# Performance work log

Hardware: AMD Instinct MI355X
Metric: run time of the kernel (lower is better)

The kernel has to match this reference:

```python
import jax, jax.numpy as jnp
import numpy as np

N = 10000      # nodes
E = 160000     # edges
F_IN = 128     # input_dim
HID = 128      # hidden_dim = per-head channels (concat=False)
OUT = 128      # output_dim
H = 4          # heads
L = 4          # layers (all 128->128 here, so params stack)


def setup_inputs() -> dict:
    key = jax.random.key(0)
    ks = jax.random.split(key, 12)
    x = jax.random.normal(ks[0], (N, F_IN), dtype=jnp.float32)
    edge_index = jax.random.randint(ks[1], (2, E), 0, N, dtype=jnp.int64)
    s = 1.0 / np.sqrt(F_IN)
    Wq = jax.random.normal(ks[2], (L, F_IN, H * HID), dtype=jnp.float32) * s
    bq = jnp.zeros((L, H * HID), dtype=jnp.float32)
    Wk = jax.random.normal(ks[3], (L, F_IN, H * HID), dtype=jnp.float32) * s
    bk = jnp.zeros((L, H * HID), dtype=jnp.float32)
    Wv = jax.random.normal(ks[4], (L, F_IN, H * HID), dtype=jnp.float32) * s
    bv = jnp.zeros((L, H * HID), dtype=jnp.float32)
    Wskip = jax.random.normal(ks[5], (L, F_IN, HID), dtype=jnp.float32) * s
    bskip = jnp.zeros((L, HID), dtype=jnp.float32)
    return {"x": x, "edge_index": edge_index, "Wq": Wq, "bq": bq,
            "Wk": Wk, "bk": bk, "Wv": Wv, "bv": bv,
            "Wskip": Wskip, "bskip": bskip}


def _transformer_conv(x, src, dst, Wq, bq, Wk, bk, Wv, bv, Ws, bs):
    # PyG TransformerConv, concat=False (mean over heads), root_weight=True
    n = x.shape[0]
    q = (x @ Wq + bq).reshape(n, H, HID)
    k = (x @ Wk + bk).reshape(n, H, HID)
    v = (x @ Wv + bv).reshape(n, H, HID)
    # per-edge attention logits: [E, H]
    alpha = jnp.einsum('ehc,ehc->eh', q[dst], k[src]) / jnp.sqrt(jnp.float32(HID))
    # segment softmax over destination node
    m = jax.ops.segment_max(alpha, dst, num_segments=n)          # [N, H]
    e = jnp.exp(alpha - m[dst])                                  # [E, H]
    z = jax.ops.segment_sum(e, dst, num_segments=n)              # [N, H]
    a = e / z[dst]                                               # [E, H]
    msg = a[:, :, None] * v[src]                                 # [E, H, C]
    out = jax.ops.segment_sum(msg, dst, num_segments=n)          # [N, H, C]
    out = out.mean(axis=1)                                       # concat=False
    return out + x @ Ws + bs                                     # skip (root_weight)


def reference(x, edge_index, Wq, bq, Wk, bk, Wv, bv, Wskip, bskip):
    src = edge_index[0]
    dst = edge_index[1]
    h = x
    for l in range(L - 1):
        h = _transformer_conv(h, src, dst, Wq[l], bq[l], Wk[l], bk[l],
                              Wv[l], bv[l], Wskip[l], bskip[l])
        h = jax.nn.relu(h)  # dropout p in eval/reference is identity
    h = _transformer_conv(h, src, dst, Wq[-1], bq[-1], Wk[-1], bk[-1],
                          Wv[-1], bv[-1], Wskip[-1], bskip[-1])
    return h
```

## Files before the change

### kernel.cpp

```cpp
#include <hip/hip_runtime.h>
#include <math.h>

static constexpr int F  = 128;
static constexpr int H  = 4;
static constexpr int HF = 512;
static constexpr int NCP = 640;
static constexpr int LAYERS = 4;

typedef __attribute__((ext_vector_type(8))) short bf16x8;
typedef __attribute__((ext_vector_type(4))) float f32x4;

__device__ __forceinline__ unsigned short f2bf(float f) {
    union { float f; unsigned u; } v; v.f = f;
    unsigned r = (v.u + 0x7FFFu + ((v.u >> 16) & 1u)) >> 16;
    return (unsigned short)r;
}
__device__ __forceinline__ float bf2f(unsigned short b) {
    union { unsigned u; float f; } v; v.u = ((unsigned)b) << 16;
    return v.f;
}

__device__ __forceinline__ float row16_sum(float x) {
    int t;
    t = __builtin_amdgcn_update_dpp(0, __float_as_int(x), 0xB1, 0xF, 0xF, true);
    x += __int_as_float(t);
    t = __builtin_amdgcn_update_dpp(0, __float_as_int(x), 0x4E, 0xF, 0xF, true);
    x += __int_as_float(t);
    t = __builtin_amdgcn_update_dpp(0, __float_as_int(x), 0x124, 0xF, 0xF, true);
    x += __int_as_float(t);
    t = __builtin_amdgcn_update_dpp(0, __float_as_int(x), 0x128, 0xF, 0xF, true);
    x += __int_as_float(t);
    return x;
}

__global__ void hist_kernel(const int* __restrict__ dst, int* __restrict__ deg, int E) {
    int e = blockIdx.x * blockDim.x + threadIdx.x;
    if (e < E) atomicAdd(&deg[dst[e]], 1);
}

__global__ void scan_kernel(const int* __restrict__ deg, int* __restrict__ row_ptr, int n) {
    __shared__ int wsum[16];
    __shared__ int carry_s, wtot_s;
    const int tid = threadIdx.x;
    const int lane = tid & 63;
    const int wid = tid >> 6;
    if (tid == 0) { carry_s = 0; row_ptr[0] = 0; }
    __syncthreads();
    for (int base = 0; base < n; base += 1024) {
        int i = base + tid;
        int x = (i < n) ? deg[i] : 0;
#pragma unroll
        for (int off = 1; off < 64; off <<= 1) {
            int t = __shfl_up(x, off, 64);
            if (lane >= off) x += t;
        }
        if (lane == 63) wsum[wid] = x;
        __syncthreads();
        if (tid == 0) {
            int s = 0;
#pragma unroll
            for (int j = 0; j < 16; ++j) { int t = wsum[j]; wsum[j] = s; s += t; }
            wtot_s = s;
        }
        __syncthreads();
        int incl = x + wsum[wid] + carry_s;
        if (i < n) row_ptr[i + 1] = incl;
        __syncthreads();
        if (tid == 0) carry_s += wtot_s;
        __syncthreads();
    }
}

__global__ void scatter_kernel(const int* __restrict__ src, const int* __restrict__ dst,
                               const int* __restrict__ row_ptr, int* __restrict__ cursor,
                               int* __restrict__ csr_src, int E) {
    int e = blockIdx.x * blockDim.x + threadIdx.x;
    if (e < E) {
        int d = dst[e];
        int pos = atomicAdd(&cursor[d], 1);
        csr_src[row_ptr[d] + pos] = src[e];
    }
}

static constexpr int NB_CONV  = 1250;
static constexpr int NB_WQK   = 64;
static constexpr int NB_WS    = 64;
static constexpr int NB_BPOST = 256;
static constexpr int NB_BIAS  = LAYERS;
static constexpr int NB_PREP  = NB_CONV + NB_WQK + NB_WS + NB_BPOST + NB_BIAS;

__global__ __launch_bounds__(256) void prep_kernel(
    const float* __restrict__ x, unsigned short* __restrict__ h_bf, int n4,
    const float* __restrict__ Wq, const float* __restrict__ Wk,
    const float* __restrict__ Wv, const float* __restrict__ Ws,
    const float* __restrict__ bq, const float* __restrict__ bs, const float* __restrict__ bv,
    unsigned short* __restrict__ Bpre, unsigned short* __restrict__ Bpost,
    float* __restrict__ biasPre, float* __restrict__ biasPost, float scale)
{
    __shared__ __attribute__((aligned(16))) float smem[64 * 33 * 2];
    const int tid = threadIdx.x;
    int b = blockIdx.x;

    if (b < NB_CONV) {
        int i = b * 256 + tid;
        if (i < n4) {
            float4 v = *(const float4*)(x + (size_t)i * 4);
            ushort4 o;
            o.x = f2bf(v.x); o.y = f2bf(v.y); o.z = f2bf(v.z); o.w = f2bf(v.w);
            *(ushort4*)(h_bf + (size_t)i * 4) = o;
        }
        return;
    }
    b -= NB_CONV;
    if (b < NB_WQK) {
        float (*As)[33] = (float (*)[33])smem;
        float (*Bs)[33] = (float (*)[33])(smem + 64 * 33);
        const int bx = b & 1, by = (b >> 1) & 1, lh = b >> 2;
        const int l = lh >> 2, h = lh & 3;
        const int c0 = by * 64, k0 = bx * 64;
        const float* Ab = Wk + (size_t)l * 65536 + h * 128;
        const float* Bb = Wq + (size_t)l * 65536 + h * 128;
        const int tx = tid & 15, ty = tid >> 4;
        float acc[4][4] = {};
        for (int jj = 0; jj < 128; jj += 32) {
#pragma unroll
            for (int rep = 0; rep < 2; ++rep) {
                int f = tid + rep * 256;
                int r = f >> 3, j4 = (f & 7) * 4;
                float4 a = *(const float4*)(Ab + (size_t)(c0 + r) * 512 + jj + j4);
                As[r][j4 + 0] = a.x; As[r][j4 + 1] = a.y; As[r][j4 + 2] = a.z; As[r][j4 + 3] = a.w;
                float4 bb = *(const float4*)(Bb + (size_t)(k0 + r) * 512 + jj + j4);
                Bs[r][j4 + 0] = bb.x; Bs[r][j4 + 1] = bb.y; Bs[r][j4 + 2] = bb.z; Bs[r][j4 + 3] = bb.w;
            }
            __syncthreads();
#pragma unroll
            for (int j = 0; j < 32; ++j) {
                float a0 = As[ty * 4 + 0][j], a1 = As[ty * 4 + 1][j];
                float a2 = As[ty * 4 + 2][j], a3 = As[ty * 4 + 3][j];
                float b0 = Bs[tx * 4 + 0][j], b1 = Bs[tx * 4 + 1][j];
                float b2 = Bs[tx * 4 + 2][j], b3 = Bs[tx * 4 + 3][j];
                acc[0][0] += a0 * b0; acc[0][1] += a0 * b1; acc[0][2] += a0 * b2; acc[0][3] += a0 * b3;
                acc[1][0] += a1 * b0; acc[1][1] += a1 * b1; acc[1][2] += a1 * b2; acc[1][3] += a1 * b3;
                acc[2][0] += a2 * b0; acc[2][1] += a2 * b1; acc[2][2] += a2 * b2; acc[2][3] += a2 * b3;
                acc[3][0] += a3 * b0; acc[3][1] += a3 * b1; acc[3][2] += a3 * b2; acc[3][3] += a3 * b3;
            }
            __syncthreads();
        }
#pragma unroll
        for (int i = 0; i < 4; ++i)
#pragma unroll
            for (int t = 0; t < 4; ++t) {
                int c = c0 + ty * 4 + i;
                int k = k0 + tx * 4 + t;
                Bpre[(size_t)l * NCP * 128 + (size_t)(h * 128 + c) * 128 + k] = f2bf(scale * acc[i][t]);
            }
        return;
    }
    b -= NB_WQK;
    if (b < NB_WS) {
        unsigned short (*t)[33] = (unsigned short (*)[33])smem;
        const int bx = b & 3, by = (b >> 2) & 3, l = b >> 4;
        const int k0 = bx * 32, n0 = by * 32;
        const int cx = tid & 31, ry = tid >> 5;
#pragma unroll
        for (int rr = 0; rr < 32; rr += 8) {
            int k = k0 + ry + rr;
            t[ry + rr][cx] = f2bf(Ws[(size_t)l * 16384 + (size_t)k * 128 + n0 + cx]);
        }
        __syncthreads();
#pragma unroll
        for (int rr = 0; rr < 32; rr += 8) {
            int n = n0 + ry + rr;
            Bpre[(size_t)l * NCP * 128 + (size_t)(512 + n) * 128 + k0 + cx] = t[cx][ry + rr];
        }
        return;
    }
    b -= NB_WS;
    if (b < NB_BPOST) {
        unsigned short (*t)[33] = (unsigned short (*)[33])smem;
        const int bx = b & 3, by = (b >> 2) & 3, lh = b >> 4;
        const int l = lh >> 2, h = lh & 3;
        const int ci0 = bx * 32, co0 = by * 32;
        const int cx = tid & 31, ry = tid >> 5;
#pragma unroll
        for (int rr = 0; rr < 32; rr += 8) {
            int ci = ci0 + ry + rr;
            t[ry + rr][cx] = f2bf(0.25f * Wv[(size_t)l * 65536 + (size_t)ci * 512 + h * 128 + co0 + cx]);
        }
        __syncthreads();
#pragma unroll
        for (int rr = 0; rr < 32; rr += 8) {
            int co = co0 + ry + rr;
            Bpost[(size_t)l * 65536 + (size_t)co * 512 + h * 128 + ci0 + cx] = t[cx][ry + rr];
        }
        return;
    }
    b -= NB_BPOST;
    {
        const int l = b;
        for (int n = tid; n < NCP; n += 256) {
            float v;
            if (n < 512) {
                int h = n >> 7, c = n & 127;
                float s = 0.f;
                for (int j = 0; j < 128; ++j)
                    s += bq[(size_t)l * 512 + h * 128 + j] * Wk[(size_t)l * 65536 + (size_t)c * 512 + h * 128 + j];
                v = s * scale;
            } else {
                v = bs[(size_t)l * 128 + (n - 512)];
            }
            biasPre[(size_t)l * NCP + n] = v;
        }
        for (int c = tid; c < 128; c += 256) {
            float s = 0.f;
            for (int h = 0; h < 4; ++h) s += bv[(size_t)l * 512 + h * 128 + c];
            biasPost[(size_t)l * 128 + c] = 0.25f * s;
        }
    }
}

__global__ __launch_bounds__(256) void gemm_pre(
    const unsigned short* __restrict__ Abf,
    const unsigned short* __restrict__ Bt,
    const float* __restrict__ bias,
    unsigned short* __restrict__ Qt,
    float* __restrict__ Sb,
    int M)
{
    __shared__ unsigned short As[128][72];
    __shared__ unsigned short Bs[128][72];

    const int tid = threadIdx.x;
    const int wave = tid >> 6, lane = tid & 63;
    const int lane16 = lane & 15, quad = lane >> 4;
    const int wr = wave >> 1, wc = wave & 1;
    const int row0 = blockIdx.y * 128;
    const int col0 = blockIdx.x * 128;

    f32x4 acc[4][4] = {};

    for (int kk = 0; kk < 128; kk += 64) {
#pragma unroll
        for (int j = 0; j < 4; ++j) {
            int c = tid + j * 256;
            int r = c >> 3, c8 = (c & 7) * 8;
            bf16x8 v = {};
            if (row0 + r < M) v = *(const bf16x8*)(Abf + (size_t)(row0 + r) * 128 + kk + c8);
            *(bf16x8*)&As[r][c8] = v;
        }
#pragma unroll
        for (int j = 0; j < 4; ++j) {
            int c = tid + j * 256;
            int r = c >> 3, c8 = (c & 7) * 8;
            *(bf16x8*)&Bs[r][c8] = *(const bf16x8*)(Bt + (size_t)(col0 + r) * 128 + kk + c8);
        }
        __syncthreads();

#pragma unroll
        for (int ks = 0; ks < 2; ++ks) {
            bf16x8 a[4], b[4];
#pragma unroll
            for (int i = 0; i < 4; ++i)
                a[i] = *(const bf16x8*)&As[wr * 64 + i * 16 + lane16][ks * 32 + quad * 8];
#pragma unroll
            for (int i = 0; i < 4; ++i)
                b[i] = *(const bf16x8*)&Bs[wc * 64 + i * 16 + lane16][ks * 32 + quad * 8];
#pragma unroll
            for (int mi = 0; mi < 4; ++mi)
#pragma unroll
                for (int ni = 0; ni < 4; ++ni)
                    acc[mi][ni] = __builtin_amdgcn_mfma_f32_16x16x32_bf16(
                        a[mi], b[ni], acc[mi][ni], 0, 0, 0);
        }
        __syncthreads();
    }

#pragma unroll
    for (int mi = 0; mi < 4; ++mi) {
        int rowb = row0 + wr * 64 + mi * 16 + quad * 4;
#pragma unroll
        for (int ni = 0; ni < 4; ++ni) {
            int col = col0 + wc * 64 + ni * 16 + lane16;
            float bv = bias[col];
#pragma unroll
            for (int r = 0; r < 4; ++r) {
                int gr = rowb + r;
                if (gr < M) {
                    float v = acc[mi][ni][r] + bv;
                    if (col < 512) Qt[(size_t)gr * 512 + col] = f2bf(v);
                    else           Sb[(size_t)gr * 128 + (col - 512)] = v;
                }
            }
        }
    }
}

__global__ __launch_bounds__(256, 4) void attn_agg(
    const unsigned short* __restrict__ Qt,
    const unsigned short* __restrict__ Hb,
    const int* __restrict__ row_ptr,
    const int* __restrict__ csr_src,
    unsigned short* __restrict__ Agg,
    int N)
{
    const int tid = threadIdx.x;
    const int wave = tid >> 6;
    const int g = (tid >> 4) & 3;
    const int l16 = tid & 15;
    const int node = blockIdx.x * 4 + wave;
    if (node >= N) return;

    const float NEG = -3e38f;

    float qf[8];
    {
        bf16x8 qv = *(const bf16x8*)(Qt + (size_t)node * HF + g * F + l16 * 8);
#pragma unroll
        for (int j = 0; j < 8; ++j) qf[j] = bf2f((unsigned short)qv[j]);
    }
    const unsigned short* Hl = Hb + (size_t)l16 * 8;

    const int beg = row_ptr[node];
    const int end = row_ptr[node + 1];

    float m = NEG, z = 0.f;
    float acc[8];
#pragma unroll
    for (int j = 0; j < 8; ++j) acc[j] = 0.f;

    if (end > beg) {
        const int last = end - 1;
        const int NB = (end - beg + 3) >> 2;

#define CLD(i) csr_src[(i) < last ? (i) : last]

        int a0 = CLD(beg + 0), a1 = CLD(beg + 1), a2 = CLD(beg + 2), a3 = CLD(beg + 3);
        bf16x8 hA0 = *(const bf16x8*)(Hl + (size_t)a0 * F);
        bf16x8 hA1 = *(const bf16x8*)(Hl + (size_t)a1 * F);
        bf16x8 hA2 = *(const bf16x8*)(Hl + (size_t)a2 * F);
        bf16x8 hA3 = *(const bf16x8*)(Hl + (size_t)a3 * F);
        int b0 = CLD(beg + 4), b1 = CLD(beg + 5), b2 = CLD(beg + 6), b3 = CLD(beg + 7);
        bf16x8 hB0 = *(const bf16x8*)(Hl + (size_t)b0 * F);
        bf16x8 hB1 = *(const bf16x8*)(Hl + (size_t)b1 * F);
        bf16x8 hB2 = *(const bf16x8*)(Hl + (size_t)b2 * F);
        bf16x8 hB3 = *(const bf16x8*)(Hl + (size_t)b3 * F);
        a0 = CLD(beg + 8);  a1 = CLD(beg + 9);  a2 = CLD(beg + 10); a3 = CLD(beg + 11);
        b0 = CLD(beg + 12); b1 = CLD(beg + 13); b2 = CLD(beg + 14); b3 = CLD(beg + 15);
        __builtin_amdgcn_sched_barrier(0);

#define ATTN_BATCH(H0, H1, H2, H3, I0, I1, I2, I3)                              \
    {                                                                           \
        float hf[4][8];                                                         \
        _Pragma("unroll")                                                       \
        for (int j = 0; j < 8; ++j) {                                           \
            hf[0][j] = bf2f((unsigned short)H0[j]);                             \
            hf[1][j] = bf2f((unsigned short)H1[j]);                             \
            hf[2][j] = bf2f((unsigned short)H2[j]);                             \
            hf[3][j] = bf2f((unsigned short)H3[j]);                             \
        }                                                                       \
        if (k + 2 < NB) {                                                       \
            H0 = *(const bf16x8*)(Hl + (size_t)I0 * F);                         \
            H1 = *(const bf16x8*)(Hl + (size_t)I1 * F);                         \
            H2 = *(const bf16x8*)(Hl + (size_t)I2 * F);                         \
            H3 = *(const bf16x8*)(Hl + (size_t)I3 * F);                         \
            I0 = CLD(base + 16); I1 = CLD(base + 17);                           \
            I2 = CLD(base + 18); I3 = CLD(base + 19);                           \
        }                                                                       \
        __builtin_amdgcn_sched_barrier(0);   \
        float p0 = 0.f, p1 = 0.f, p2 = 0.f, p3 = 0.f;                           \
        _Pragma("unroll")                                                       \
        for (int j = 0; j < 8; ++j) {                                           \
            p0 += qf[j] * hf[0][j]; p1 += qf[j] * hf[1][j];                     \
            p2 += qf[j] * hf[2][j]; p3 += qf[j] * hf[3][j];                     \
        }                                                                       \
        p0 = row16_sum(p0); p1 = row16_sum(p1);                                 \
        p2 = row16_sum(p2); p3 = row16_sum(p3);                                 \
        const int nv = end - base;                                              \
        if (nv < 4) { if (nv < 2) p1 = NEG; if (nv < 3) p2 = NEG; p3 = NEG; }   \
        float bm = fmaxf(fmaxf(p0, p1), fmaxf(p2, p3));                         \
        float mn = fmaxf(m, bm);                                                \
        float rs = exp2f(m - mn);                                               \
        float w0 = exp2f(p0 - mn), w1 = exp2f(p1 - mn);                         \
        float w2 = exp2f(p2 - mn), w3 = exp2f(p3 - mn);                         \
        z = z * rs + (w0 + w1) + (w2 + w3);                                     \
        _Pragma("unroll")                                                       \
        for (int j = 0; j < 8; ++j)                                             \
            acc[j] = acc[j] * rs + w0 * hf[0][j] + w1 * hf[1][j]                \
                   + w2 * hf[2][j] + w3 * hf[3][j];                             \
        m = mn;                                                                 \
    }

        int base = beg;
        int k = 0;
        for (;;) {
            ATTN_BATCH(hA0, hA1, hA2, hA3, a0, a1, a2, a3)
            ++k; base += 4;
            if (k >= NB) break;
            ATTN_BATCH(hB0, hB1, hB2, hB3, b0, b1, b2, b3)
            ++k; base += 4;
            if (k >= NB) break;
        }
#undef ATTN_BATCH
#undef CLD
    }

    float inv = (z > 0.f) ? 1.f / z : 0.f;
    bf16x8 o;
#pragma unroll
    for (int j = 0; j < 8; ++j) o[j] = (short)f2bf(acc[j] * inv);
    *(bf16x8*)(Agg + (size_t)node * HF + g * F + l16 * 8) = o;
}

__global__ __launch_bounds__(256) void gemm_post(
    const unsigned short* __restrict__ Agg,
    const unsigned short* __restrict__ Bt,
    const float* __restrict__ bias,
    const float* __restrict__ Sb,
    float* __restrict__ out_f,
    unsigned short* __restrict__ out_bf,
    int relu, int M)
{
    __shared__ unsigned short As[64][72];
    __shared__ unsigned short Bs[64][72];

    const int tid = threadIdx.x;
    const int wave = tid >> 6, lane = tid & 63;
    const int lane16 = lane & 15, quad = lane >> 4;
    const int row0 = blockIdx.y * 64;
    const int col0 = blockIdx.x * 64;

    f32x4 acc[4] = {};

    for (int kk = 0; kk < 512; kk += 64) {
#pragma unroll
        for (int rep = 0; rep < 2; ++rep) {
            int c = tid + rep * 256;
            int r = c >> 3, c8 = (c & 7) * 8;
            bf16x8 v = {};
            if (row0 + r < M) v = *(const bf16x8*)(Agg + (size_t)(row0 + r) * 512 + kk + c8);
            *(bf16x8*)&As[r][c8] = v;
            *(bf16x8*)&Bs[r][c8] = *(const bf16x8*)(Bt + (size_t)(col0 + r) * 512 + kk + c8);
        }
        __syncthreads();

#pragma unroll
        for (int ks = 0; ks < 2; ++ks) {
            bf16x8 b = *(const bf16x8*)&Bs[wave * 16 + lane16][ks * 32 + quad * 8];
#pragma unroll
            for (int mt = 0; mt < 4; ++mt) {
                bf16x8 a = *(const bf16x8*)&As[mt * 16 + lane16][ks * 32 + quad * 8];
                acc[mt] = __builtin_amdgcn_mfma_f32_16x16x32_bf16(a, b, acc[mt], 0, 0, 0);
            }
        }
        __syncthreads();
    }

    const int col = col0 + wave * 16 + lane16;
    const float bcol = bias[col];
#pragma unroll
    for (int mt = 0; mt < 4; ++mt) {
#pragma unroll
        for (int r = 0; r < 4; ++r) {
            int row = row0 + mt * 16 + quad * 4 + r;
            if (row < M) {
                float v = acc[mt][r] + bcol + Sb[(size_t)row * 128 + col];
                if (relu) v = fmaxf(v, 0.f);
                if (out_f)  out_f[(size_t)row * 128 + col] = v;
                if (out_bf) out_bf[(size_t)row * 128 + col] = f2bf(v);
            }
        }
    }
}

extern "C" void kernel_launch(void* const* d_in, const int* in_sizes, int n_in,
                              void* d_out, int out_size, void* d_ws, size_t ws_size,
                              hipStream_t stream) {
    const float* x     = (const float*)d_in[0];
    const int*   ei    = (const int*)d_in[1];
    const float* Wq    = (const float*)d_in[2];
    const float* bq    = (const float*)d_in[3];
    const float* Wk    = (const float*)d_in[4];
    const float* bk    = (const float*)d_in[5];
    const float* Wv    = (const float*)d_in[6];
    const float* bv    = (const float*)d_in[7];
    const float* Wskip = (const float*)d_in[8];
    const float* bskip = (const float*)d_in[9];
    float* out = (float*)d_out;
    (void)bk;

    const int N = in_sizes[0] / F;
    const int E = in_sizes[1] / 2;
    const float scale = 0.08838834764831845f * 1.4426950408889634f;

    const int* src = ei;
    const int* dst = ei + E;

    char* p = (char*)d_ws;
    float* Sb       = (float*)p;               p += (size_t)N * F * sizeof(float);
    float* biasPreP = (float*)p;               p += (size_t)LAYERS * NCP * sizeof(float);
    float* biasPostP= (float*)p;               p += (size_t)LAYERS * 128 * sizeof(float);
    unsigned short* h_bf  = (unsigned short*)p; p += (size_t)N * F * sizeof(unsigned short);
    unsigned short* Qt    = (unsigned short*)p; p += (size_t)N * HF * sizeof(unsigned short);
    unsigned short* AggB  = (unsigned short*)p; p += (size_t)N * HF * sizeof(unsigned short);
    unsigned short* BpreP = (unsigned short*)p; p += (size_t)LAYERS * NCP * 128 * sizeof(unsigned short);
    unsigned short* BpostP= (unsigned short*)p; p += (size_t)LAYERS * 128 * 512 * sizeof(unsigned short);
    int* deg     = (int*)p;                    p += (size_t)N * sizeof(int);
    int* cursor  = (int*)p;                    p += (size_t)N * sizeof(int);
    int* row_ptr = (int*)p;                    p += (size_t)(N + 1) * sizeof(int);
    int* csr_src = (int*)p;

    hipMemsetAsync(deg, 0, 2 * (size_t)N * sizeof(int), stream);
    {
        int blocks = (E + 255) / 256;
        hist_kernel<<<blocks, 256, 0, stream>>>(dst, deg, E);
        scan_kernel<<<1, 1024, 0, stream>>>(deg, row_ptr, N);
        scatter_kernel<<<blocks, 256, 0, stream>>>(src, dst, row_ptr, cursor, csr_src, E);
    }

    prep_kernel<<<NB_PREP, 256, 0, stream>>>(x, h_bf, N * F / 4,
                                             Wq, Wk, Wv, Wskip,
                                             bq, bskip, bv,
                                             BpreP, BpostP, biasPreP, biasPostP, scale);

    const int rowBlocks128 = (N + 127) / 128;
    const int rowBlocks64  = (N + 63) / 64;
    const int attnBlocks   = (N + 3) / 4;

    for (int l = 0; l < LAYERS; ++l) {
        dim3 gridPre(NCP / 128, rowBlocks128);
        gemm_pre<<<gridPre, 256, 0, stream>>>(h_bf,
                                              BpreP + (size_t)l * NCP * 128,
                                              biasPreP + (size_t)l * NCP,
                                              Qt, Sb, N);

        attn_agg<<<attnBlocks, 256, 0, stream>>>(Qt, h_bf, row_ptr, csr_src, AggB, N);

        float* out_f = nullptr;
        unsigned short* out_bf = nullptr;
        int relu;
        if (l == LAYERS - 1) { out_f = out; relu = 0; }
        else { out_bf = h_bf; relu = 1; }

        dim3 gridPost(2, rowBlocks64);
        gemm_post<<<gridPost, 256, 0, stream>>>(AggB,
                                                BpostP + (size_t)l * 128 * 512,
                                                biasPostP + (size_t)l * 128,
                                                Sb, out_f, out_bf, relu, N);
    }
}
```

Baseline: 265.3 us.

## Split each node's edge list across two waves and merge softmax partials in LDS

The attention aggregation kernel now assigns one node per 128-thread block, and its two waves process interleaved 4-edge batches of the node's neighbor list. Each wave keeps its own online-softmax state (max, sum, accumulator). Wave 1 writes its partial state to shared memory and wave 0 merges the two with rescaling before writing the output. This halves the serial edge chain per wave to cut latency on the gather loop. The cost is a block barrier, LDS traffic, many more small blocks, and duplicated Q loads and prologue work per node.

```diff
diff --git a/kernel.cpp b/kernel.cpp
--- a/kernel.cpp
+++ b/kernel.cpp
@@ -295,7 +295,7 @@
     }
 }
 
-__global__ __launch_bounds__(256, 4) void attn_agg(
+__global__ __launch_bounds__(128, 4) void attn_agg(
     const unsigned short* __restrict__ Qt,
     const unsigned short* __restrict__ Hb,
     const int* __restrict__ row_ptr,
@@ -303,12 +303,13 @@
     unsigned short* __restrict__ Agg,
     int N)
 {
+    __shared__ float part[4][16][10];
+
     const int tid = threadIdx.x;
-    const int wave = tid >> 6;
-    const int g = (tid >> 4) & 3;
+    const int wv  = tid >> 6;
+    const int g   = (tid >> 4) & 3;
     const int l16 = tid & 15;
-    const int node = blockIdx.x * 4 + wave;
-    if (node >= N) return;
+    const int node = blockIdx.x;
 
     const float NEG = -3e38f;
 
@@ -328,24 +329,25 @@
 #pragma unroll
     for (int j = 0; j < 8; ++j) acc[j] = 0.f;
 
-    if (end > beg) {
+    const int begw = beg + wv * 4;
+    if (begw < end) {
         const int last = end - 1;
-        const int NB = (end - beg + 3) >> 2;
+        const int NB = (end - begw + 7) >> 3;
 
 #define CLD(i) csr_src[(i) < last ? (i) : last]
 
-        int a0 = CLD(beg + 0), a1 = CLD(beg + 1), a2 = CLD(beg + 2), a3 = CLD(beg + 3);
+        int a0 = CLD(begw + 0), a1 = CLD(begw + 1), a2 = CLD(begw + 2), a3 = CLD(begw + 3);
         bf16x8 hA0 = *(const bf16x8*)(Hl + (size_t)a0 * F);
         bf16x8 hA1 = *(const bf16x8*)(Hl + (size_t)a1 * F);
         bf16x8 hA2 = *(const bf16x8*)(Hl + (size_t)a2 * F);
         bf16x8 hA3 = *(const bf16x8*)(Hl + (size_t)a3 * F);
-        int b0 = CLD(beg + 4), b1 = CLD(beg + 5), b2 = CLD(beg + 6), b3 = CLD(beg + 7);
+        int b0 = CLD(begw + 8), b1 = CLD(begw + 9), b2 = CLD(begw + 10), b3 = CLD(begw + 11);
         bf16x8 hB0 = *(const bf16x8*)(Hl + (size_t)b0 * F);
         bf16x8 hB1 = *(const bf16x8*)(Hl + (size_t)b1 * F);
         bf16x8 hB2 = *(const bf16x8*)(Hl + (size_t)b2 * F);
         bf16x8 hB3 = *(const bf16x8*)(Hl + (size_t)b3 * F);
-        a0 = CLD(beg + 8);  a1 = CLD(beg + 9);  a2 = CLD(beg + 10); a3 = CLD(beg + 11);
-        b0 = CLD(beg + 12); b1 = CLD(beg + 13); b2 = CLD(beg + 14); b3 = CLD(beg + 15);
+        a0 = CLD(begw + 16); a1 = CLD(begw + 17); a2 = CLD(begw + 18); a3 = CLD(begw + 19);
+        b0 = CLD(begw + 24); b1 = CLD(begw + 25); b2 = CLD(begw + 26); b3 = CLD(begw + 27);
         __builtin_amdgcn_sched_barrier(0);
 
 #define ATTN_BATCH(H0, H1, H2, H3, I0, I1, I2, I3)                              \
@@ -363,8 +365,8 @@
             H1 = *(const bf16x8*)(Hl + (size_t)I1 * F);                         \
             H2 = *(const bf16x8*)(Hl + (size_t)I2 * F);                         \
             H3 = *(const bf16x8*)(Hl + (size_t)I3 * F);                         \
-            I0 = CLD(base + 16); I1 = CLD(base + 17);                           \
-            I2 = CLD(base + 18); I3 = CLD(base + 19);                           \
+            I0 = CLD(base + 32); I1 = CLD(base + 33);                           \
+            I2 = CLD(base + 34); I3 = CLD(base + 35);                           \
         }                                                                       \
         __builtin_amdgcn_sched_barrier(0);   \
         float p0 = 0.f, p1 = 0.f, p2 = 0.f, p3 = 0.f;                           \
@@ -390,25 +392,41 @@
         m = mn;                                                                 \
     }
 
-        int base = beg;
+        int base = begw;
         int k = 0;
         for (;;) {
             ATTN_BATCH(hA0, hA1, hA2, hA3, a0, a1, a2, a3)
-            ++k; base += 4;
+            ++k; base += 8;
             if (k >= NB) break;
             ATTN_BATCH(hB0, hB1, hB2, hB3, b0, b1, b2, b3)
-            ++k; base += 4;
+            ++k; base += 8;
             if (k >= NB) break;
         }
 #undef ATTN_BATCH
 #undef CLD
     }
 
-    float inv = (z > 0.f) ? 1.f / z : 0.f;
-    bf16x8 o;
-#pragma unroll
-    for (int j = 0; j < 8; ++j) o[j] = (short)f2bf(acc[j] * inv);
-    *(bf16x8*)(Agg + (size_t)node * HF + g * F + l16 * 8) = o;
+    if (wv == 1) {
+#pragma unroll
+        for (int j = 0; j < 8; ++j) part[g][l16][j] = acc[j];
+        part[g][l16][8] = m;
+        part[g][l16][9] = z;
+    }
+    __syncthreads();
+    if (wv == 0) {
+        float om = part[g][l16][8];
+        float oz = part[g][l16][9];
+        float M  = fmaxf(m, om);
+        float sa = exp2f(m - M);
+        float sb = exp2f(om - M);
+        float zz = z * sa + oz * sb;
+        float inv = (zz > 0.f) ? 1.f / zz : 0.f;
+        bf16x8 o;
+#pragma unroll
+        for (int j = 0; j < 8; ++j)
+            o[j] = (short)f2bf((acc[j] * sa + part[g][l16][j] * sb) * inv);
+        *(bf16x8*)(Agg + (size_t)node * HF + g * F + l16 * 8) = o;
+    }
 }
 
 __global__ __launch_bounds__(256) void gemm_post(
@@ -524,7 +542,6 @@
 
     const int rowBlocks128 = (N + 127) / 128;
     const int rowBlocks64  = (N + 63) / 64;
-    const int attnBlocks   = (N + 3) / 4;
 
     for (int l = 0; l < LAYERS; ++l) {
         dim3 gridPre(NCP / 128, rowBlocks128);
@@ -533,7 +550,7 @@
                                               biasPreP + (size_t)l * NCP,
                                               Qt, Sb, N);
 
-        attn_agg<<<attnBlocks, 256, 0, stream>>>(Qt, h_bf, row_ptr, csr_src, AggB, N);
+        attn_agg<<<N, 128, 0, stream>>>(Qt, h_bf, row_ptr, csr_src, AggB, N);
 
         float* out_f = nullptr;
         unsigned short* out_bf = nullptr;
```

Measured after the change: 264.2 us. Within noise of the previous version (-0.4%).
